# Kernel optimization log

Measured on AMD Instinct MI355X. Metric: run time of the kernel, lower is better.

## Reference

```python
import jax, jax.numpy as jnp
import numpy as np

OUT, IN, BLK, RANK = 4096, 4096, 32, 16
N_BLOCKS = IN // BLK  # 128
Q_ZERO = 128.0  # center of unsigned code range, maps codes to signed values


def setup_inputs() -> dict:
    key = jax.random.key(0)
    ks = jax.random.split(key, 6)
    x = jax.random.normal(ks[0], (4, 2048, IN), dtype=jnp.float32)
    # GGML-style block-quantized weight: int codes in blocks of 32 + per-block fp scale
    q_weight = jax.random.randint(ks[1], (OUT, N_BLOCKS, BLK), 0, 256, dtype=jnp.int32)
    scales = jax.random.uniform(ks[2], (OUT, N_BLOCKS), dtype=jnp.float32) * 0.02
    # LoRA patch applied to dequantized weight
    lora_up = jax.random.normal(ks[3], (OUT, RANK), dtype=jnp.float32) * 0.02
    lora_down = jax.random.normal(ks[4], (RANK, IN), dtype=jnp.float32) * 0.02
    bias = jax.random.normal(ks[5], (OUT,), dtype=jnp.float32)
    return {"x": x, "q_weight": q_weight, "scales": scales,
            "lora_up": lora_up, "lora_down": lora_down, "bias": bias}


def reference(x, q_weight, scales, lora_up, lora_down, bias):
    # 1) dequantize: per-block scale * centered int codes -> full fp weight [OUT, IN]
    w = (q_weight.astype(jnp.float32) - Q_ZERO) * scales[:, :, None]
    w = w.reshape(OUT, IN)
    # 2) apply LoRA patch to the dequantized weight (patch function in get_weight)
    w = w + lora_up @ lora_down
    # 3) delegate to the linear forward operation: y = x @ W^T + b
    return jnp.einsum('bsd,od->bso', x, w) + bias
```

## Files before the change

### kernel.cpp

```cpp
#include <hip/hip_runtime.h>
#include <cstdint>
#include <cstddef>

#define M_TOT 8192
#define N_TOT 4096
#define K_TOT 4096
#define RANK  16
#define BM 128
#define BN 128
#define BK 32

typedef float f32x4 __attribute__((ext_vector_type(4)));
typedef __bf16 bf16x8 __attribute__((ext_vector_type(8)));
typedef unsigned short u16x8 __attribute__((ext_vector_type(8)));

__device__ __forceinline__ unsigned short f32_to_bf16(float f) {
    union { float f; uint32_t u; } v; v.f = f;
    uint32_t r = v.u + (0x7fffu + ((v.u >> 16) & 1u));
    return (unsigned short)(r >> 16);
}

__device__ __forceinline__ void gload_lds16(const void* g, void* l) {
    __builtin_amdgcn_global_load_lds(
        (const __attribute__((address_space(1))) void*)g,
        (__attribute__((address_space(3))) void*)l,
        16, 0, 0);
}

__global__ __launch_bounds__(256) void convert_x_kernel(const float* __restrict__ x,
                                                        unsigned short* __restrict__ xb,
                                                        int n8) {
    int i = blockIdx.x * 256 + threadIdx.x;
    if (i >= n8) return;
    float4 a = ((const float4*)x)[2 * (size_t)i];
    float4 b = ((const float4*)x)[2 * (size_t)i + 1];
    u16x8 o;
    o[0] = f32_to_bf16(a.x); o[1] = f32_to_bf16(a.y);
    o[2] = f32_to_bf16(a.z); o[3] = f32_to_bf16(a.w);
    o[4] = f32_to_bf16(b.x); o[5] = f32_to_bf16(b.y);
    o[6] = f32_to_bf16(b.z); o[7] = f32_to_bf16(b.w);
    *(u16x8*)&xb[(size_t)i * 8] = o;
}

__global__ __launch_bounds__(256) void build_w_kernel(const int* __restrict__ q,
                                                      const float* __restrict__ scales,
                                                      const float* __restrict__ up,
                                                      const float* __restrict__ down,
                                                      unsigned short* __restrict__ W) {
    const int o0 = blockIdx.x * 4;
    const int t = threadIdx.x;
    __shared__ float u[4][RANK];
    if (t < 64) u[t >> 4][t & 15] = up[(o0 + (t >> 4)) * RANK + (t & 15)];
    __syncthreads();

#pragma unroll
    for (int cc = 0; cc < 2; cc++) {
        const int c = t + 256 * cc;
        const int k0 = c * 8;
        float acc[4][8];
#pragma unroll
        for (int row = 0; row < 4; row++) {
            const int o = o0 + row;
            int4 qa = *(const int4*)&q[(size_t)o * K_TOT + k0];
            int4 qb = *(const int4*)&q[(size_t)o * K_TOT + k0 + 4];
            const float s = scales[o * (K_TOT / 32) + (k0 >> 5)];
            acc[row][0] = (float)(qa.x - 128) * s;
            acc[row][1] = (float)(qa.y - 128) * s;
            acc[row][2] = (float)(qa.z - 128) * s;
            acc[row][3] = (float)(qa.w - 128) * s;
            acc[row][4] = (float)(qb.x - 128) * s;
            acc[row][5] = (float)(qb.y - 128) * s;
            acc[row][6] = (float)(qb.z - 128) * s;
            acc[row][7] = (float)(qb.w - 128) * s;
        }
#pragma unroll
        for (int r = 0; r < RANK; r++) {
            float4 da = *(const float4*)&down[r * K_TOT + k0];
            float4 db = *(const float4*)&down[r * K_TOT + k0 + 4];
#pragma unroll
            for (int row = 0; row < 4; row++) {
                const float ur = u[row][r];
                acc[row][0] += ur * da.x; acc[row][1] += ur * da.y;
                acc[row][2] += ur * da.z; acc[row][3] += ur * da.w;
                acc[row][4] += ur * db.x; acc[row][5] += ur * db.y;
                acc[row][6] += ur * db.z; acc[row][7] += ur * db.w;
            }
        }
#pragma unroll
        for (int row = 0; row < 4; row++) {
            u16x8 o8;
#pragma unroll
            for (int j = 0; j < 8; j++) o8[j] = f32_to_bf16(acc[row][j]);
            *(u16x8*)&W[(size_t)(o0 + row) * K_TOT + k0] = o8;
        }
    }
}

__global__ __launch_bounds__(256) void gemm_bt_kernel(const unsigned short* __restrict__ A,
                                                      const unsigned short* __restrict__ B,
                                                      const float* __restrict__ bias,
                                                      float* __restrict__ C) {
    __shared__ unsigned short As[BM * BK];
    __shared__ unsigned short Bs[BN * BK];

    const int tid  = threadIdx.x;
    const int wave = tid >> 6;
    const int lane = tid & 63;
    const int wm = wave >> 1;
    const int wn = wave & 1;

    const int tile_m = (int)blockIdx.y * BM;
    const int tile_n = (int)blockIdx.x * BN;

    const int lrow = lane >> 2;
    const int lcol = ((lane & 3) ^ ((lrow >> 1) & 3)) * 8;

    const int quad = lane >> 4;
    const int l16  = lane & 15;
    const int swz  = (l16 >> 1) & 3;

    f32x4 acc[4][4];
#pragma unroll
    for (int i = 0; i < 4; i++)
#pragma unroll
        for (int j = 0; j < 4; j++) {
            f32x4 z = {0.f, 0.f, 0.f, 0.f};
            acc[i][j] = z;
        }

    for (int k0 = 0; k0 < K_TOT; k0 += BK) {
#pragma unroll
        for (int j = 0; j < 2; j++) {
            const int r0 = (j * 4 + wave) * 16;
            gload_lds16(A + (size_t)(tile_m + r0 + lrow) * K_TOT + (k0 + lcol), &As[r0 * BK]);
            gload_lds16(B + (size_t)(tile_n + r0 + lrow) * K_TOT + (k0 + lcol), &Bs[r0 * BK]);
        }
        __syncthreads();

        const int slot = (quad ^ swz) * 8;
        bf16x8 af[4], bfr[4];
#pragma unroll
        for (int mi = 0; mi < 4; mi++)
            af[mi] = *(const bf16x8*)&As[(wm * 64 + mi * 16 + l16) * BK + slot];
#pragma unroll
        for (int ni = 0; ni < 4; ni++)
            bfr[ni] = *(const bf16x8*)&Bs[(wn * 64 + ni * 16 + l16) * BK + slot];

#pragma unroll
        for (int mi = 0; mi < 4; mi++)
#pragma unroll
            for (int ni = 0; ni < 4; ni++)
                acc[mi][ni] = __builtin_amdgcn_mfma_f32_16x16x32_bf16(af[mi], bfr[ni], acc[mi][ni], 0, 0, 0);
        __syncthreads();
    }

#pragma unroll
    for (int ni = 0; ni < 4; ni++) {
        const int col = tile_n + wn * 64 + ni * 16 + l16;
        const float bv = bias[col];
#pragma unroll
        for (int mi = 0; mi < 4; mi++) {
#pragma unroll
            for (int r = 0; r < 4; r++) {
                const int row = tile_m + wm * 64 + mi * 16 + quad * 4 + r;
                C[(size_t)row * N_TOT + col] = acc[mi][ni][r] + bv;
            }
        }
    }
}

extern "C" void kernel_launch(void* const* d_in, const int* in_sizes, int n_in,
                              void* d_out, int out_size, void* d_ws, size_t ws_size,
                              hipStream_t stream) {
    const float* x      = (const float*)d_in[0];
    const int*   q      = (const int*)d_in[1];
    const float* scales = (const float*)d_in[2];
    const float* up     = (const float*)d_in[3];
    const float* down   = (const float*)d_in[4];
    const float* bias   = (const float*)d_in[5];
    float* out = (float*)d_out;

    unsigned short* xb = (unsigned short*)d_ws;
    unsigned short* wb = xb + (size_t)M_TOT * K_TOT;

    const int n8 = M_TOT * K_TOT / 8;
    convert_x_kernel<<<n8 / 256, 256, 0, stream>>>(x, xb, n8);
    build_w_kernel<<<N_TOT / 4, 256, 0, stream>>>(q, scales, up, down, wb);
    gemm_bt_kernel<<<dim3(N_TOT / BN, M_TOT / BM), 256, 0, stream>>>(xb, wb, bias, out);
}
```

Baseline: 587.7 us.

## Rewrite GEMM as 256x256 double-buffered tile with 8 waves and staged prefetch

The bf16 GEMM moves from a 128x128x32 single-buffered tile with 4 waves to a 256x256x64 tile with 8 waves. LDS is double-buffered, and global-to-LDS loads for the next K step are interleaved with MFMA phases under explicit vmcnt waits, raw barriers and s_setprio. Block indices are remapped so neighbouring blocks share tiles in cache. The aim is more reuse per byte loaded and hiding memory latency behind MFMA work, at the cost of more registers and LDS per block and hand-scheduled synchronisation that is fragile.

```diff
diff --git a/kernel.cpp b/kernel.cpp
--- a/kernel.cpp
+++ b/kernel.cpp
@@ -6,9 +6,11 @@
 #define N_TOT 4096
 #define K_TOT 4096
 #define RANK  16
-#define BM 128
-#define BN 128
-#define BK 32
+
+#define BM 256
+#define BN 256
+#define BK 64
+#define NT (K_TOT / BK)
 
 typedef float f32x4 __attribute__((ext_vector_type(4)));
 typedef __bf16 bf16x8 __attribute__((ext_vector_type(8)));
@@ -96,62 +98,144 @@
     }
 }
 
-__global__ __launch_bounds__(256) void gemm_bt_kernel(const unsigned short* __restrict__ A,
-                                                      const unsigned short* __restrict__ B,
-                                                      const float* __restrict__ bias,
-                                                      float* __restrict__ C) {
-    __shared__ unsigned short As[BM * BK];
-    __shared__ unsigned short Bs[BN * BK];
-
-    const int tid  = threadIdx.x;
+#define BARRIER() do { asm volatile("" ::: "memory"); \
+                       __builtin_amdgcn_s_barrier(); \
+                       asm volatile("" ::: "memory"); } while (0)
+
+__global__ __launch_bounds__(512, 2) void gemm_bt_kernel(const unsigned short* __restrict__ A,
+                                                         const unsigned short* __restrict__ B,
+                                                         const float* __restrict__ bias,
+                                                         float* __restrict__ C) {
+    __shared__ unsigned short As[2][2][128 * BK];
+    __shared__ unsigned short Bs[2][2][128 * BK];
+
+    const int tid  = (int)threadIdx.x;
     const int wave = tid >> 6;
     const int lane = tid & 63;
-    const int wm = wave >> 1;
-    const int wn = wave & 1;
-
-    const int tile_m = (int)blockIdx.y * BM;
-    const int tile_n = (int)blockIdx.x * BN;
-
-    const int lrow = lane >> 2;
-    const int lcol = ((lane & 3) ^ ((lrow >> 1) & 3)) * 8;
-
+    const int wm   = wave >> 2;
+    const int wn   = wave & 3;
+    const int wbh  = wn >> 1;
+    const int wbr  = (wn & 1) * 64;
+
+    int lin = (int)(blockIdx.y * gridDim.x + blockIdx.x);
+    lin = (lin & 7) * 64 + (lin >> 3);
+    const int tile_n = (lin & 15) * BN;
+    const int tile_m = (lin >> 4) * BM;
+
+    const int srow  = tid >> 3;
+    const int sk    = ((tid & 7) ^ (srow & 7)) * 8;
+    const int wbase = wave * 512;
+
+    const int l16  = lane & 15;
     const int quad = lane >> 4;
-    const int l16  = lane & 15;
-    const int swz  = (l16 >> 1) & 3;
-
-    f32x4 acc[4][4];
-#pragma unroll
-    for (int i = 0; i < 4; i++)
-#pragma unroll
-        for (int j = 0; j < 4; j++) {
-            f32x4 z = {0.f, 0.f, 0.f, 0.f};
-            acc[i][j] = z;
-        }
-
-    for (int k0 = 0; k0 < K_TOT; k0 += BK) {
-#pragma unroll
-        for (int j = 0; j < 2; j++) {
-            const int r0 = (j * 4 + wave) * 16;
-            gload_lds16(A + (size_t)(tile_m + r0 + lrow) * K_TOT + (k0 + lcol), &As[r0 * BK]);
-            gload_lds16(B + (size_t)(tile_n + r0 + lrow) * K_TOT + (k0 + lcol), &Bs[r0 * BK]);
-        }
-        __syncthreads();
-
-        const int slot = (quad ^ swz) * 8;
-        bf16x8 af[4], bfr[4];
-#pragma unroll
-        for (int mi = 0; mi < 4; mi++)
-            af[mi] = *(const bf16x8*)&As[(wm * 64 + mi * 16 + l16) * BK + slot];
-#pragma unroll
-        for (int ni = 0; ni < 4; ni++)
-            bfr[ni] = *(const bf16x8*)&Bs[(wn * 64 + ni * 16 + l16) * BK + slot];
-
-#pragma unroll
-        for (int mi = 0; mi < 4; mi++)
-#pragma unroll
-            for (int ni = 0; ni < 4; ni++)
-                acc[mi][ni] = __builtin_amdgcn_mfma_f32_16x16x32_bf16(af[mi], bfr[ni], acc[mi][ni], 0, 0, 0);
-        __syncthreads();
+    const int sw   = l16 & 7;
+    const int slot0 = ((quad ^ sw) * 8);
+    const int slot1 = (((4 + quad) ^ sw) * 8);
+
+    const unsigned short* aBase = A + (size_t)(tile_m + srow) * K_TOT + sk;
+    const unsigned short* bBase = B + (size_t)(tile_n + srow) * K_TOT + sk;
+
+#define STAGE_A(d, h, t) do { \
+    gload_lds16(aBase + (size_t)((h) * 128) * K_TOT + (size_t)(t) * BK, &As[d][h][wbase]); \
+    gload_lds16(aBase + (size_t)((h) * 128 + 64) * K_TOT + (size_t)(t) * BK, &As[d][h][4096 + wbase]); \
+  } while (0)
+#define STAGE_B(d, h, t) do { \
+    gload_lds16(bBase + (size_t)((h) * 128) * K_TOT + (size_t)(t) * BK, &Bs[d][h][wbase]); \
+    gload_lds16(bBase + (size_t)((h) * 128 + 64) * K_TOT + (size_t)(t) * BK, &Bs[d][h][4096 + wbase]); \
+  } while (0)
+
+    f32x4 acc[8][4];
+#pragma unroll
+    for (int i = 0; i < 8; i++)
+#pragma unroll
+        for (int j = 0; j < 4; j++) { f32x4 z = {0.f, 0.f, 0.f, 0.f}; acc[i][j] = z; }
+
+    STAGE_A(0, 0, 0); STAGE_A(0, 1, 0);
+    STAGE_B(0, 0, 0); STAGE_B(0, 1, 0);
+    STAGE_A(1, 0, 1); STAGE_A(1, 1, 1);
+    asm volatile("s_waitcnt vmcnt(4)" ::: "memory");
+    BARRIER();
+
+    for (int t = 0; t < NT; ++t) {
+        const int cur = t & 1, nxt = cur ^ 1;
+        const unsigned short* Ah = &As[cur][wm][l16 * BK];
+        const unsigned short* Bh = &Bs[cur][wbh][(wbr + l16) * BK];
+
+        bf16x8 af[4][2], bfA[2][2], bfB[2][2];
+
+        if (t + 1 < NT) STAGE_B(nxt, 0, t + 1);
+#pragma unroll
+        for (int mi = 0; mi < 4; mi++) {
+            af[mi][0] = *(const bf16x8*)&Ah[(mi * 16) * BK + slot0];
+            af[mi][1] = *(const bf16x8*)&Ah[(mi * 16) * BK + slot1];
+        }
+#pragma unroll
+        for (int ni = 0; ni < 2; ni++) {
+            bfA[ni][0] = *(const bf16x8*)&Bh[(ni * 16) * BK + slot0];
+            bfA[ni][1] = *(const bf16x8*)&Bh[(ni * 16) * BK + slot1];
+        }
+        BARRIER();
+        __builtin_amdgcn_s_setprio(1);
+#pragma unroll
+        for (int mi = 0; mi < 4; mi++)
+#pragma unroll
+            for (int ni = 0; ni < 2; ni++) {
+                acc[mi][ni] = __builtin_amdgcn_mfma_f32_16x16x32_bf16(af[mi][0], bfA[ni][0], acc[mi][ni], 0, 0, 0);
+                acc[mi][ni] = __builtin_amdgcn_mfma_f32_16x16x32_bf16(af[mi][1], bfA[ni][1], acc[mi][ni], 0, 0, 0);
+            }
+        __builtin_amdgcn_s_setprio(0);
+        BARRIER();
+
+        if (t + 1 < NT) STAGE_B(nxt, 1, t + 1);
+#pragma unroll
+        for (int ni = 0; ni < 2; ni++) {
+            bfB[ni][0] = *(const bf16x8*)&Bh[((ni + 2) * 16) * BK + slot0];
+            bfB[ni][1] = *(const bf16x8*)&Bh[((ni + 2) * 16) * BK + slot1];
+        }
+        BARRIER();
+        __builtin_amdgcn_s_setprio(1);
+#pragma unroll
+        for (int mi = 0; mi < 4; mi++)
+#pragma unroll
+            for (int ni = 0; ni < 2; ni++) {
+                acc[mi][ni + 2] = __builtin_amdgcn_mfma_f32_16x16x32_bf16(af[mi][0], bfB[ni][0], acc[mi][ni + 2], 0, 0, 0);
+                acc[mi][ni + 2] = __builtin_amdgcn_mfma_f32_16x16x32_bf16(af[mi][1], bfB[ni][1], acc[mi][ni + 2], 0, 0, 0);
+            }
+        __builtin_amdgcn_s_setprio(0);
+        BARRIER();
+
+#pragma unroll
+        for (int mi = 0; mi < 4; mi++) {
+            af[mi][0] = *(const bf16x8*)&Ah[((mi + 4) * 16) * BK + slot0];
+            af[mi][1] = *(const bf16x8*)&Ah[((mi + 4) * 16) * BK + slot1];
+        }
+        BARRIER();
+        __builtin_amdgcn_s_setprio(1);
+#pragma unroll
+        for (int mi = 0; mi < 4; mi++)
+#pragma unroll
+            for (int ni = 0; ni < 2; ni++) {
+                acc[mi + 4][ni + 2] = __builtin_amdgcn_mfma_f32_16x16x32_bf16(af[mi][0], bfB[ni][0], acc[mi + 4][ni + 2], 0, 0, 0);
+                acc[mi + 4][ni + 2] = __builtin_amdgcn_mfma_f32_16x16x32_bf16(af[mi][1], bfB[ni][1], acc[mi + 4][ni + 2], 0, 0, 0);
+            }
+        __builtin_amdgcn_s_setprio(0);
+        BARRIER();
+
+        if (t + 2 < NT) { STAGE_A(cur, 0, t + 2); STAGE_A(cur, 1, t + 2); }
+        __builtin_amdgcn_s_setprio(1);
+#pragma unroll
+        for (int mi = 0; mi < 4; mi++)
+#pragma unroll
+            for (int ni = 0; ni < 2; ni++) {
+                acc[mi + 4][ni] = __builtin_amdgcn_mfma_f32_16x16x32_bf16(af[mi][0], bfA[ni][0], acc[mi + 4][ni], 0, 0, 0);
+                acc[mi + 4][ni] = __builtin_amdgcn_mfma_f32_16x16x32_bf16(af[mi][1], bfA[ni][1], acc[mi + 4][ni], 0, 0, 0);
+            }
+        __builtin_amdgcn_s_setprio(0);
+        if (t + 1 < NT) {
+            if (t + 2 < NT) asm volatile("s_waitcnt vmcnt(4)" ::: "memory");
+            else            asm volatile("s_waitcnt vmcnt(0)" ::: "memory");
+        }
+        BARRIER();
     }
 
 #pragma unroll
@@ -159,14 +243,16 @@
         const int col = tile_n + wn * 64 + ni * 16 + l16;
         const float bv = bias[col];
 #pragma unroll
-        for (int mi = 0; mi < 4; mi++) {
+        for (int mi = 0; mi < 8; mi++) {
 #pragma unroll
             for (int r = 0; r < 4; r++) {
-                const int row = tile_m + wm * 64 + mi * 16 + quad * 4 + r;
+                const int row = tile_m + wm * 128 + mi * 16 + quad * 4 + r;
                 C[(size_t)row * N_TOT + col] = acc[mi][ni][r] + bv;
             }
         }
     }
+#undef STAGE_A
+#undef STAGE_B
 }
 
 extern "C" void kernel_launch(void* const* d_in, const int* in_sizes, int n_in,
@@ -186,5 +272,5 @@
     const int n8 = M_TOT * K_TOT / 8;
     convert_x_kernel<<<n8 / 256, 256, 0, stream>>>(x, xb, n8);
     build_w_kernel<<<N_TOT / 4, 256, 0, stream>>>(q, scales, up, down, wb);
-    gemm_bt_kernel<<<dim3(N_TOT / BN, M_TOT / BM), 256, 0, stream>>>(xb, wb, bias, out);
-}
+    gemm_bt_kernel<<<dim3(N_TOT / BN, M_TOT / BM), 512, 0, stream>>>(xb, wb, bias, out);
+}
```

Result: slower. 614.3 us (+4.5%).
